# Optimization experiments

Hardware: AMD Instinct MI355X
Metric: run time of the kernel (lower is better)

Reference implementation:

```python
import jax, jax.numpy as jnp
import numpy as np

N_NODES = 50000
N_EDGES = 800000
D = 128


def setup_inputs() -> dict:
    key = jax.random.key(0)
    k1, k2, k3, k4 = jax.random.split(key, 4)
    x = jax.random.normal(k1, (N_NODES, D), dtype=jnp.float32)
    src = jax.random.randint(k2, (N_EDGES,), 0, N_NODES, dtype=jnp.int64)
    dst = jax.random.randint(k3, (N_EDGES,), 0, N_NODES, dtype=jnp.int64)
    # nn.Linear(D, D, bias=False): weight shape [out, in]
    W = jax.random.normal(k4, (D, D), dtype=jnp.float32) * (1.0 / np.sqrt(D))
    return {"x": x, "src": src, "dst": dst, "W": W}


def reference(x, src, dst, W):
    h_in = x
    # update_all(copy_src, reduce_sum): gather src features, segment-sum over dst
    agg = jax.ops.segment_sum(x[src], dst, num_segments=N_NODES)  # [N, D]
    h = agg @ W.T                 # Linear(bias=False)
    h = jax.nn.relu(h)            # activation
    h = h + h_in                  # residual (is_normalize=False)
    return h
```

## Files before the change

kernel.cpp:

```cpp
#include <hip/hip_runtime.h>
#include <hip/hip_bf16.h>

#define N_NODES 50000
#define N_EDGES 800000
#define D 128

#define NBUCK 3125
#define NREP  4
#define RCAP  192
#define NMAX  768

#define CONV_BLOCKS 3200

using bf16x8 = __attribute__((ext_vector_type(8))) short;
using u16x8  = __attribute__((ext_vector_type(8))) unsigned short;
using f32x4  = __attribute__((ext_vector_type(4))) float;

static __device__ __forceinline__ ushort f2bf(float f) {
    __hip_bfloat16 h = __float2bfloat16(f);
    return *reinterpret_cast<ushort*>(&h);
}
static __device__ __forceinline__ float bf2f(ushort u) {
    return __uint_as_float(((unsigned)u) << 16);
}


__global__ void __launch_bounds__(256)
convert_scatter(const float4* __restrict__ x4, ushort* __restrict__ xb,
                const float* __restrict__ W, ushort* __restrict__ wb,
                const int* __restrict__ src, const int* __restrict__ dst,
                int* __restrict__ bcnt, int* __restrict__ pairs) {
    const int gt  = blockIdx.x * 256 + threadIdx.x;
    const int rep = blockIdx.x & (NREP - 1);

    if (gt < 2048) {
        int o  = gt & 127;
        int kc = gt >> 7;
        const float4* wp = (const float4*)(W + (size_t)o * D + kc * 8);
        float4 w0 = wp[0], w1 = wp[1];
        bf16x8 hv;
        hv[0] = (short)f2bf(w0.x); hv[1] = (short)f2bf(w0.y);
        hv[2] = (short)f2bf(w0.z); hv[3] = (short)f2bf(w0.w);
        hv[4] = (short)f2bf(w1.x); hv[5] = (short)f2bf(w1.y);
        hv[6] = (short)f2bf(w1.z); hv[7] = (short)f2bf(w1.w);
        *(bf16x8*)&wb[gt * 8] = hv;
    }

    if (gt < N_EDGES / 4) {
        int4 s = ((const int4*)src)[gt];
        int4 d = ((const int4*)dst)[gt];
#pragma unroll
        for (int e = 0; e < 4; ++e) {
            int sv = (e == 0) ? s.x : (e == 1) ? s.y : (e == 2) ? s.z : s.w;
            int dv = (e == 0) ? d.x : (e == 1) ? d.y : (e == 2) ? d.z : d.w;
            int seg = (dv >> 4) * NREP + rep;
            int pos = atomicAdd(&bcnt[seg * 16], 1);
            if (pos < RCAP)
                pairs[seg * RCAP + pos] = sv | ((dv & 15) << 16);
        }
    }

    const int total4 = N_NODES * D / 4;
    const int stride = CONV_BLOCKS * 256;
    for (int j = gt; j < total4; j += stride) {
        float4 v = x4[j];
        ushort4 u = make_ushort4(f2bf(v.x), f2bf(v.y), f2bf(v.z), f2bf(v.w));
        *(ushort4*)(xb + (size_t)j * 4) = u;
    }
}

__global__ void __launch_bounds__(256)
csr_gather_gemm(const int* __restrict__ pairs, const int* __restrict__ bcnt,
                const ushort* __restrict__ xb, const ushort* __restrict__ wb,
                float* __restrict__ out) {
    __shared__ __align__(16) char lds[14592];
    ushort* lsrc  = (ushort*)lds;
    ushort* aggL  = (ushort*)(lds + 1600);
    float*  Ew    = (float*)(lds + 5952);
    int*    lcnt2 = (int*)(lds + 14400);
    int*    lcur  = (int*)(lds + 14464);
    int*    lbeg  = (int*)(lds + 14528);

    const int b    = blockIdx.x;
    const int tid  = threadIdx.x;
    const int lane = tid & 63;
    const int wv   = tid >> 6;
    const int m16  = lane & 15;
    const int q    = lane >> 4;

    const int pb = b * NREP;
    int c0 = bcnt[(pb + 0) * 16]; if (c0 > RCAP) c0 = RCAP;
    int c1 = bcnt[(pb + 1) * 16]; if (c1 > RCAP) c1 = RCAP;
    int c2 = bcnt[(pb + 2) * 16]; if (c2 > RCAP) c2 = RCAP;
    int c3 = bcnt[(pb + 3) * 16]; if (c3 > RCAP) c3 = RCAP;
    const int s1 = c0 + c1, s2 = s1 + c2, n = s2 + c3;

    int p0 = -1, p1 = -1, p2 = -1;
#pragma unroll
    for (int k = 0; k < 3; ++k) {
        int i = tid + k * 256;
        if (i < n) {
            int rep, off;
            if      (i < c0) { rep = 0; off = i; }
            else if (i < s1) { rep = 1; off = i - c0; }
            else if (i < s2) { rep = 2; off = i - s1; }
            else             { rep = 3; off = i - s2; }
            int p = pairs[(pb + rep) * RCAP + off];
            if (k == 0) p0 = p; else if (k == 1) p1 = p; else p2 = p;
        }
    }

    if (tid < 16) lcnt2[tid] = 0;
    __syncthreads();
    if (p0 >= 0) atomicAdd(&lcnt2[p0 >> 16], 1);
    if (p1 >= 0) atomicAdd(&lcnt2[p1 >> 16], 1);
    if (p2 >= 0) atomicAdd(&lcnt2[p2 >> 16], 1);
    __syncthreads();
    if (tid < 16) {
        int v = lcnt2[tid];
        int incl = v;
#pragma unroll
        for (int o = 1; o < 16; o <<= 1) {
            int t = __shfl_up(incl, o, 64);
            if (tid >= o) incl += t;
        }
        lbeg[tid] = incl - v;
        lcur[tid] = incl - v;
    }
    __syncthreads();
    if (p0 >= 0) { int pos = atomicAdd(&lcur[p0 >> 16], 1); lsrc[pos] = (ushort)(p0 & 0xFFFF); }
    if (p1 >= 0) { int pos = atomicAdd(&lcur[p1 >> 16], 1); lsrc[pos] = (ushort)(p1 & 0xFFFF); }
    if (p2 >= 0) { int pos = atomicAdd(&lcur[p2 >> 16], 1); lsrc[pos] = (ushort)(p2 & 0xFFFF); }
    __syncthreads();

    const int c8 = m16 << 3;
    const ushort* xbb = xb + c8;

    auto drain = [&](int t, int e, float* acc) {
        for (; t + 8 <= e; t += 8) {
            int s0 = lsrc[t + q];
            int s1v = lsrc[t + 4 + q];
            u16x8 u0 = *(const u16x8*)(xbb + (size_t)s0 * D);
            u16x8 u1 = *(const u16x8*)(xbb + (size_t)s1v * D);
#pragma unroll
            for (int j = 0; j < 8; ++j) acc[j] += bf2f(u0[j]) + bf2f(u1[j]);
        }
        for (; t + 4 <= e; t += 4) {
            int s = lsrc[t + q];
            u16x8 u = *(const u16x8*)(xbb + (size_t)s * D);
#pragma unroll
            for (int j = 0; j < 8; ++j) acc[j] += bf2f(u[j]);
        }
        const int rem = e - t;
        if (rem && q < rem) {
            int s = lsrc[t + q];
            u16x8 u = *(const u16x8*)(xbb + (size_t)s * D);
#pragma unroll
            for (int j = 0; j < 8; ++j) acc[j] += bf2f(u[j]);
        }
    };
    auto red_store = [&](int nloc, float* acc) {
#pragma unroll
        for (int j = 0; j < 8; ++j) {
            acc[j] += __shfl_xor(acc[j], 16, 64);
            acc[j] += __shfl_xor(acc[j], 32, 64);
        }
        if (q == 0) {
            u16x8 u;
#pragma unroll
            for (int j = 0; j < 8; ++j) u[j] = f2bf(acc[j]);
            *(u16x8*)&aggL[(size_t)nloc * 136 + c8] = u;
        }
    };

#pragma unroll 1
    for (int pm = 0; pm < 2; ++pm) {
        const int nA = wv * 4 + pm * 2;
        const int nB = nA + 1;
        int tA = lbeg[nA]; const int eA = lcur[nA];
        int tB = lbeg[nB]; const int eB = lcur[nB];
        float accA[8], accB[8];
#pragma unroll
        for (int j = 0; j < 8; ++j) { accA[j] = 0.f; accB[j] = 0.f; }

        while (tA + 8 <= eA && tB + 8 <= eB) {
            int a0 = lsrc[tA + q], a1 = lsrc[tA + 4 + q];
            int b0 = lsrc[tB + q], b1 = lsrc[tB + 4 + q];
            u16x8 uA0 = *(const u16x8*)(xbb + (size_t)a0 * D);
            u16x8 uA1 = *(const u16x8*)(xbb + (size_t)a1 * D);
            u16x8 uB0 = *(const u16x8*)(xbb + (size_t)b0 * D);
            u16x8 uB1 = *(const u16x8*)(xbb + (size_t)b1 * D);
#pragma unroll
            for (int j = 0; j < 8; ++j) {
                accA[j] += bf2f(uA0[j]) + bf2f(uA1[j]);
                accB[j] += bf2f(uB0[j]) + bf2f(uB1[j]);
            }
            tA += 8; tB += 8;
        }
        while (tA + 4 <= eA && tB + 4 <= eB) {
            int a0 = lsrc[tA + q], b0 = lsrc[tB + q];
            u16x8 uA = *(const u16x8*)(xbb + (size_t)a0 * D);
            u16x8 uB = *(const u16x8*)(xbb + (size_t)b0 * D);
#pragma unroll
            for (int j = 0; j < 8; ++j) {
                accA[j] += bf2f(uA[j]);
                accB[j] += bf2f(uB[j]);
            }
            tA += 4; tB += 4;
        }
        drain(tA, eA, accA);
        drain(tB, eB, accB);
        red_store(nA, accA);
        red_store(nB, accB);
    }
    __syncthreads();

    bf16x8 a[4];
#pragma unroll
    for (int kb = 0; kb < 4; ++kb)
        a[kb] = *(const bf16x8*)&aggL[(size_t)m16 * 136 + kb * 32 + q * 8];

    f32x4 acc[2];
#pragma unroll
    for (int tt = 0; tt < 2; ++tt) {
        const int t = wv * 2 + tt;
        acc[tt] = (f32x4){0.f, 0.f, 0.f, 0.f};
#pragma unroll
        for (int kb = 0; kb < 4; ++kb) {
            bf16x8 bfr = *(const bf16x8*)&wb[(((kb * 4 + q) * 128) + t * 16 + m16) * 8];
            acc[tt] = __builtin_amdgcn_mfma_f32_16x16x32_bf16(a[kb], bfr, acc[tt], 0, 0, 0);
        }
    }

#pragma unroll
    for (int tt = 0; tt < 2; ++tt) {
        const int t = wv * 2 + tt;
#pragma unroll
        for (int r = 0; r < 4; ++r)
            Ew[(q * 4 + r) * 132 + t * 16 + m16] = acc[tt][r];
    }
    __syncthreads();

#pragma unroll
    for (int k = 0; k < 2; ++k) {
        int idx = tid + k * 256;
        int row = idx >> 5;
        int c4  = (idx & 31) << 2;
        int node = b * 16 + row;
        float4 v  = *(const float4*)&Ew[row * 132 + c4];
        ushort4 xu = *(const ushort4*)(xb + (size_t)node * D + c4);
        float4 o;
        o.x = fmaxf(v.x, 0.f) + bf2f(xu.x);
        o.y = fmaxf(v.y, 0.f) + bf2f(xu.y);
        o.z = fmaxf(v.z, 0.f) + bf2f(xu.z);
        o.w = fmaxf(v.w, 0.f) + bf2f(xu.w);
        *(float4*)(out + (size_t)node * D + c4) = o;
    }
}

__global__ void zero_out(float4* __restrict__ p, int n4) {
    int i = blockIdx.x * 256 + threadIdx.x;
    if (i < n4) p[i] = make_float4(0.f, 0.f, 0.f, 0.f);
}
__global__ void scatter_edges(const float* __restrict__ x,
                              const int* __restrict__ src,
                              const int* __restrict__ dst,
                              float* __restrict__ agg) {
    long long tid = (long long)blockIdx.x * 256 + threadIdx.x;
    if (tid >= (long long)N_EDGES * 32) return;
    int edge = (int)(tid >> 5);
    int c    = ((int)tid & 31) << 2;
    const float4 v = *(const float4*)(x + (size_t)src[edge] * D + c);
    float* p = agg + (size_t)dst[edge] * D + c;
    unsafeAtomicAdd(p + 0, v.x);
    unsafeAtomicAdd(p + 1, v.y);
    unsafeAtomicAdd(p + 2, v.z);
    unsafeAtomicAdd(p + 3, v.w);
}
__global__ void __launch_bounds__(256)
gemm_relu_res_f32(float* data, const float* __restrict__ W,
                  const float* __restrict__ x) {
    __shared__ __align__(16) char lds[50176];
    ushort* Wl = (ushort*)lds;
    ushort* Al = (ushort*)(lds + 32768);
    const int tid  = threadIdx.x;
    const int lane = tid & 63;
    const int wv   = tid >> 6;
    const int m16  = lane & 15;
    const int q    = lane >> 4;
#pragma unroll
    for (int i = 0; i < 8; ++i) {
        int g  = tid + i * 256;
        int o  = g & 127;
        int kc = g >> 7;
        const float4* wp = (const float4*)(W + (size_t)o * D + kc * 8);
        float4 w0 = wp[0], w1 = wp[1];
        bf16x8 hv;
        hv[0] = (short)f2bf(w0.x); hv[1] = (short)f2bf(w0.y);
        hv[2] = (short)f2bf(w0.z); hv[3] = (short)f2bf(w0.w);
        hv[4] = (short)f2bf(w1.x); hv[5] = (short)f2bf(w1.y);
        hv[6] = (short)f2bf(w1.z); hv[7] = (short)f2bf(w1.w);
        *(bf16x8*)&Wl[g * 8] = hv;
    }
    __syncthreads();
    const int nb = blockIdx.x * 64 + wv * 16;
    ushort* Aw = &Al[wv * (16 * 136)];
#pragma unroll
    for (int m = 0; m < 16; ++m) {
        int node = nb + m;
        float2 v = make_float2(0.f, 0.f);
        if (node < N_NODES)
            v = *(const float2*)(data + (size_t)node * D + lane * 2);
        *(ushort2*)&Aw[m * 136 + lane * 2] = make_ushort2(f2bf(v.x), f2bf(v.y));
    }
    bf16x8 a[4];
#pragma unroll
    for (int kb = 0; kb < 4; ++kb)
        a[kb] = *(const bf16x8*)&Aw[m16 * 136 + kb * 32 + q * 8];
    f32x4 acc[8];
#pragma unroll
    for (int t = 0; t < 8; ++t) {
        acc[t] = (f32x4){0.f, 0.f, 0.f, 0.f};
#pragma unroll
        for (int kb = 0; kb < 4; ++kb) {
            bf16x8 bfr = *(const bf16x8*)&Wl[(((kb * 4 + q) * 128) + t * 16 + m16) * 8];
            acc[t] = __builtin_amdgcn_mfma_f32_16x16x32_bf16(a[kb], bfr, acc[t], 0, 0, 0);
        }
    }
    __syncthreads();
    float* Ew = (float*)(lds + wv * 8448);
#pragma unroll
    for (int t = 0; t < 8; ++t)
#pragma unroll
        for (int r = 0; r < 4; ++r)
            Ew[(q * 4 + r) * 132 + t * 16 + m16] = acc[t][r];
    const int h  = lane >> 5;
    const int c4 = (lane & 31) << 2;
#pragma unroll
    for (int j = 0; j < 8; ++j) {
        int r = j * 2 + h;
        int node = nb + r;
        if (node < N_NODES) {
            float4 v  = *(const float4*)&Ew[r * 132 + c4];
            float4 xi = *(const float4*)(x + (size_t)node * D + c4);
            float4 o;
            o.x = fmaxf(v.x, 0.f) + xi.x;
            o.y = fmaxf(v.y, 0.f) + xi.y;
            o.z = fmaxf(v.z, 0.f) + xi.z;
            o.w = fmaxf(v.w, 0.f) + xi.w;
            *(float4*)(data + (size_t)node * D + c4) = o;
        }
    }
}

extern "C" void kernel_launch(void* const* d_in, const int* in_sizes, int n_in,
                              void* d_out, int out_size, void* d_ws, size_t ws_size,
                              hipStream_t stream) {
    const float* x   = (const float*)d_in[0];
    const int*   src = (const int*)d_in[1];
    const int*   dst = (const int*)d_in[2];
    const float* W   = (const float*)d_in[3];
    float* out = (float*)d_out;

    char* ws = (char*)d_ws;
    int*    bcnt  = (int*)ws;        ws += (size_t)NBUCK * NREP * 64;
    int*    pairs = (int*)ws;        ws += (size_t)NBUCK * NREP * RCAP * 4;
    ushort* xb    = (ushort*)ws;     ws += (size_t)N_NODES * D * 2;
    ushort* wb    = (ushort*)ws;     ws += (size_t)D * D * 2;
    const bool big_ws = (ws_size >= (size_t)(ws - (char*)d_ws));

    if (big_ws) {
        hipMemsetAsync(bcnt, 0, (size_t)NBUCK * NREP * 64, stream);
        convert_scatter<<<CONV_BLOCKS, 256, 0, stream>>>(
            (const float4*)x, xb, W, wb, src, dst, bcnt, pairs);
        csr_gather_gemm<<<NBUCK, 256, 0, stream>>>(pairs, bcnt, xb, wb, out);
    } else {
        int n4 = N_NODES * D / 4;
        zero_out<<<(n4 + 255) / 256, 256, 0, stream>>>((float4*)out, n4);
        long long n_scatter = (long long)N_EDGES * 32;
        scatter_edges<<<(int)((n_scatter + 255) / 256), 256, 0, stream>>>(
            x, src, dst, out);
        gemm_relu_res_f32<<<(N_NODES + 63) / 64, 256, 0, stream>>>(out, W, x);
    }
}
```

Before: 154.9 us.

## Bucket edges per destination node instead of per 16-node group with replicas

Replaces the 16-node buckets (with 4 replicas and an in-block counting sort) with one fixed 64-slot bucket per destination node, indexed directly by the edge's dst. The gather kernel then loads its 1024 slots straight into LDS without the local histogram, scan and reorder. The scatter kernel becomes one edge per thread with scalar loads, and the x conversion is folded into the same launch. Counter contention rises per node, the memset covers 50000 padded counters, and edges past 64 for one node would be silently dropped.

```diff
diff --git a/kernel.cpp b/kernel.cpp
--- a/kernel.cpp
+++ b/kernel.cpp
@@ -5,12 +5,10 @@
 #define N_EDGES 800000
 #define D 128
 
+#define RCAP  64
 #define NBUCK 3125
-#define NREP  4
-#define RCAP  192
-#define NMAX  768
-
-#define CONV_BLOCKS 3200
+
+#define CONV_BLOCKS (N_EDGES / 256)
 
 using bf16x8 = __attribute__((ext_vector_type(8))) short;
 using u16x8  = __attribute__((ext_vector_type(8))) unsigned short;
@@ -30,8 +28,11 @@
                 const float* __restrict__ W, ushort* __restrict__ wb,
                 const int* __restrict__ src, const int* __restrict__ dst,
                 int* __restrict__ bcnt, int* __restrict__ pairs) {
-    const int gt  = blockIdx.x * 256 + threadIdx.x;
-    const int rep = blockIdx.x & (NREP - 1);
+    const int gt = blockIdx.x * 256 + threadIdx.x;
+
+    const int sv = src[gt];
+    const int dv = dst[gt];
+    const int pos = atomicAdd(&bcnt[dv * 16], 1);
 
     if (gt < 2048) {
         int o  = gt & 127;
@@ -46,40 +47,27 @@
         *(bf16x8*)&wb[gt * 8] = hv;
     }
 
-    if (gt < N_EDGES / 4) {
-        int4 s = ((const int4*)src)[gt];
-        int4 d = ((const int4*)dst)[gt];
-#pragma unroll
-        for (int e = 0; e < 4; ++e) {
-            int sv = (e == 0) ? s.x : (e == 1) ? s.y : (e == 2) ? s.z : s.w;
-            int dv = (e == 0) ? d.x : (e == 1) ? d.y : (e == 2) ? d.z : d.w;
-            int seg = (dv >> 4) * NREP + rep;
-            int pos = atomicAdd(&bcnt[seg * 16], 1);
-            if (pos < RCAP)
-                pairs[seg * RCAP + pos] = sv | ((dv & 15) << 16);
-        }
-    }
-
-    const int total4 = N_NODES * D / 4;
-    const int stride = CONV_BLOCKS * 256;
-    for (int j = gt; j < total4; j += stride) {
+#pragma unroll
+    for (int k = 0; k < 2; ++k) {
+        int j = gt + k * N_EDGES;
         float4 v = x4[j];
         ushort4 u = make_ushort4(f2bf(v.x), f2bf(v.y), f2bf(v.z), f2bf(v.w));
         *(ushort4*)(xb + (size_t)j * 4) = u;
     }
+
+    if (pos < RCAP)
+        pairs[(dv << 6) + pos] = sv;
 }
 
 __global__ void __launch_bounds__(256)
 csr_gather_gemm(const int* __restrict__ pairs, const int* __restrict__ bcnt,
                 const ushort* __restrict__ xb, const ushort* __restrict__ wb,
                 float* __restrict__ out) {
-    __shared__ __align__(16) char lds[14592];
-    ushort* lsrc  = (ushort*)lds;
-    ushort* aggL  = (ushort*)(lds + 1600);
-    float*  Ew    = (float*)(lds + 5952);
-    int*    lcnt2 = (int*)(lds + 14400);
-    int*    lcur  = (int*)(lds + 14464);
-    int*    lbeg  = (int*)(lds + 14528);
+    __shared__ __align__(16) char lds[8448];
+    ushort* lsrc = (ushort*)lds;
+    ushort* aggL = (ushort*)(lds + 2048);
+    int*    lcnt = (int*)(lds + 6400);
+    float*  Ew   = (float*)lds;
 
     const int b    = blockIdx.x;
     const int tid  = threadIdx.x;
@@ -88,49 +76,15 @@
     const int m16  = lane & 15;
     const int q    = lane >> 4;
 
-    const int pb = b * NREP;
-    int c0 = bcnt[(pb + 0) * 16]; if (c0 > RCAP) c0 = RCAP;
-    int c1 = bcnt[(pb + 1) * 16]; if (c1 > RCAP) c1 = RCAP;
-    int c2 = bcnt[(pb + 2) * 16]; if (c2 > RCAP) c2 = RCAP;
-    int c3 = bcnt[(pb + 3) * 16]; if (c3 > RCAP) c3 = RCAP;
-    const int s1 = c0 + c1, s2 = s1 + c2, n = s2 + c3;
-
-    int p0 = -1, p1 = -1, p2 = -1;
-#pragma unroll
-    for (int k = 0; k < 3; ++k) {
+    if (tid < 16) {
+        int c = bcnt[(b * 16 + tid) * 16];
+        lcnt[tid] = (c > RCAP) ? RCAP : c;
+    }
+#pragma unroll
+    for (int k = 0; k < 4; ++k) {
         int i = tid + k * 256;
-        if (i < n) {
-            int rep, off;
-            if      (i < c0) { rep = 0; off = i; }
-            else if (i < s1) { rep = 1; off = i - c0; }
-            else if (i < s2) { rep = 2; off = i - s1; }
-            else             { rep = 3; off = i - s2; }
-            int p = pairs[(pb + rep) * RCAP + off];
-            if (k == 0) p0 = p; else if (k == 1) p1 = p; else p2 = p;
-        }
-    }
-
-    if (tid < 16) lcnt2[tid] = 0;
-    __syncthreads();
-    if (p0 >= 0) atomicAdd(&lcnt2[p0 >> 16], 1);
-    if (p1 >= 0) atomicAdd(&lcnt2[p1 >> 16], 1);
-    if (p2 >= 0) atomicAdd(&lcnt2[p2 >> 16], 1);
-    __syncthreads();
-    if (tid < 16) {
-        int v = lcnt2[tid];
-        int incl = v;
-#pragma unroll
-        for (int o = 1; o < 16; o <<= 1) {
-            int t = __shfl_up(incl, o, 64);
-            if (tid >= o) incl += t;
-        }
-        lbeg[tid] = incl - v;
-        lcur[tid] = incl - v;
-    }
-    __syncthreads();
-    if (p0 >= 0) { int pos = atomicAdd(&lcur[p0 >> 16], 1); lsrc[pos] = (ushort)(p0 & 0xFFFF); }
-    if (p1 >= 0) { int pos = atomicAdd(&lcur[p1 >> 16], 1); lsrc[pos] = (ushort)(p1 & 0xFFFF); }
-    if (p2 >= 0) { int pos = atomicAdd(&lcur[p2 >> 16], 1); lsrc[pos] = (ushort)(p2 & 0xFFFF); }
+        lsrc[i] = (ushort)(pairs[b * 1024 + i] & 0xFFFF);
+    }
     __syncthreads();
 
     const int c8 = m16 << 3;
@@ -177,8 +131,8 @@
     for (int pm = 0; pm < 2; ++pm) {
         const int nA = wv * 4 + pm * 2;
         const int nB = nA + 1;
-        int tA = lbeg[nA]; const int eA = lcur[nA];
-        int tB = lbeg[nB]; const int eB = lcur[nB];
+        int tA = nA << 6; const int eA = tA + lcnt[nA];
+        int tB = nB << 6; const int eB = tB + lcnt[nB];
         float accA[8], accB[8];
 #pragma unroll
         for (int j = 0; j < 8; ++j) { accA[j] = 0.f; accB[j] = 0.f; }
@@ -219,6 +173,7 @@
 #pragma unroll
     for (int kb = 0; kb < 4; ++kb)
         a[kb] = *(const bf16x8*)&aggL[(size_t)m16 * 136 + kb * 32 + q * 8];
+    __syncthreads();
 
     f32x4 acc[2];
 #pragma unroll
@@ -363,14 +318,14 @@
     float* out = (float*)d_out;
 
     char* ws = (char*)d_ws;
-    int*    bcnt  = (int*)ws;        ws += (size_t)NBUCK * NREP * 64;
-    int*    pairs = (int*)ws;        ws += (size_t)NBUCK * NREP * RCAP * 4;
+    int*    bcnt  = (int*)ws;        ws += (size_t)N_NODES * 64;
+    int*    pairs = (int*)ws;        ws += (size_t)N_NODES * RCAP * 4;
     ushort* xb    = (ushort*)ws;     ws += (size_t)N_NODES * D * 2;
     ushort* wb    = (ushort*)ws;     ws += (size_t)D * D * 2;
     const bool big_ws = (ws_size >= (size_t)(ws - (char*)d_ws));
 
     if (big_ws) {
-        hipMemsetAsync(bcnt, 0, (size_t)NBUCK * NREP * 64, stream);
+        hipMemsetAsync(bcnt, 0, (size_t)N_NODES * 64, stream);
         convert_scatter<<<CONV_BLOCKS, 256, 0, stream>>>(
             (const float4*)x, xb, W, wb, src, dst, bcnt, pairs);
         csr_gather_gemm<<<NBUCK, 256, 0, stream>>>(pairs, bcnt, xb, wb, out);
```

New measurement: 158.2 us. +2.2%, slower.
